# Performance work log

Hardware: AMD Instinct MI355X
Metric: run time of the kernel (lower is better)

Reference implementation:

```python
import jax, jax.numpy as jnp
import numpy as np

GROUPS = 8

def conv1d(x, w, b, stride=1, groups=1):
    # x: [B,C,L], w: [O, I//groups, K]
    y = jax.lax.conv_general_dilated(x, w, (stride,), 'VALID',
        dimension_numbers=('NCH', 'OIH', 'NCH'), feature_group_count=groups)
    return y + b[None, :, None]

def shuffle1d(x, groups):
    B, C, L = x.shape
    cpg = C // groups
    return x.reshape(B, groups, cpg, L).transpose(0, 2, 1, 3).reshape(B, C, L)

def setup_inputs() -> dict:
    key = jax.random.key(0)
    ks = jax.random.split(key, 12)
    C = 256
    B, L = 8, 4096
    g = GROUPS
    sc = 0.05
    inp = {
        'x':   jax.random.normal(ks[0], (B, C, L), dtype=jnp.float32),
        'w1':  jax.random.normal(ks[1], (C, C // g, 3), dtype=jnp.float32) * sc,
        'b1':  jax.random.normal(ks[2], (C,), dtype=jnp.float32) * sc,
        'w2':  jax.random.normal(ks[3], (C, C // g, 3), dtype=jnp.float32) * sc,
        'b2':  jax.random.normal(ks[4], (C,), dtype=jnp.float32) * sc,
        'wa1': jax.random.normal(ks[5], (C, 2 * C // g, 1), dtype=jnp.float32) * sc,
        'ba1': jax.random.normal(ks[6], (C,), dtype=jnp.float32) * sc,
        'wa2': jax.random.normal(ks[7], (C, C // g, 1), dtype=jnp.float32) * sc,
        'ba2': jax.random.normal(ks[8], (C,), dtype=jnp.float32) * sc,
        'w3':  jax.random.normal(ks[9], (C, C // g, 5), dtype=jnp.float32) * sc,  # kernel_size-4=5
        'b3':  jax.random.normal(ks[10], (C,), dtype=jnp.float32) * sc,
    }
    return inp

def reference(x, w1, b1, w2, b2, wa1, ba1, wa2, ba2, w3, b3):
    g = GROUPS
    # in_state has length 0 at init, so cat is identity; L >= kernel_size.
    h = conv1d(x, w1, b1, stride=1, groups=g)      # [B,C,L-2]
    h = shuffle1d(h, g)
    h = conv1d(h, w2, b2, stride=1, groups=g)      # [B,C,L-4]
    h = shuffle1d(h, g)
    # SortAttn: stable ascending sort over channel dim
    sorted_h = jnp.sort(h, axis=1, stable=True)
    a = conv1d(jnp.concatenate((sorted_h, h), axis=1), wa1, ba1, stride=1, groups=g)
    a = shuffle1d(a, g)
    a = jax.nn.sigmoid(conv1d(a, wa2, ba2, stride=1, groups=g))
    h = h * a
    y = conv1d(h, w3, b3, stride=1, groups=g)      # [B,C,L-8]
    return y
```

## Files before the change

### kernel.cpp

```cpp
#include <hip/hip_runtime.h>
#include <math.h>

#define BB 8
#define CCH 256
#define LLEN 4096
#define L1V 4094
#define L2V 4092
#define L3V 4088
#define NCOL (BB * L2V)

__global__ void prep_kernel(const float* __restrict__ wa1, const float* __restrict__ wa2,
                            float* __restrict__ wt1T, float* __restrict__ wt2T) {
    int i = blockIdx.x;
    int o = threadIdx.x;
    if (i < 64) {
        wt1T[i * 256 + o] = wa1[o * 64 + i];
    } else {
        int ii = i - 64;
        if (ii < 32) wt2T[ii * 256 + o] = wa2[o * 32 + ii];
    }
}

__global__ __launch_bounds__(256, 4) void conv1_kernel(const float* __restrict__ x,
                                                       const float* __restrict__ w1,
                                                       const float* __restrict__ b1,
                                                       float* __restrict__ t1) {
    __shared__ float xs[9248];
    const int b = blockIdx.y;
    const int l0 = blockIdx.x * 32;
    const int t = threadIdx.x;

#pragma unroll
    for (int j = 0; j < 9; ++j) {
        int f = t + 256 * j;
        int row = f / 9;
        int q = f - row * 9;
        size_t rb = (size_t)(b * CCH + row) * LLEN;
        float4 v;
        int base = l0 + 4 * q;
        if (base + 3 < LLEN) {
            v = *(const float4*)(x + rb + base);
        } else {
            v.x = x[rb + min(base + 0, LLEN - 1)];
            v.y = x[rb + min(base + 1, LLEN - 1)];
            v.z = x[rb + min(base + 2, LLEN - 1)];
            v.w = x[rb + min(base + 3, LLEN - 1)];
        }
        int a = row * 36 + (row >> 5) * 4 + 4 * q;
        *(float4*)&xs[a] = v;
    }
    __syncthreads();

    const int oc = t;
    const int go = t >> 5;
    float acc[32];
#pragma unroll
    for (int l = 0; l < 32; ++l) acc[l] = 0.f;

    for (int i = 0; i < 32; ++i) {
        int row = go * 32 + i;
        int base = row * 36 + go * 4;
        float wv0 = w1[oc * 96 + i * 3 + 0];
        float wv1 = w1[oc * 96 + i * 3 + 1];
        float wv2 = w1[oc * 96 + i * 3 + 2];
#pragma unroll
        for (int q = 0; q < 9; ++q) {
            float4 v = *(const float4*)&xs[base + 4 * q];
#pragma unroll
            for (int j = 0; j < 4; ++j) {
                int e = 4 * q + j;
                float xv = (&v.x)[j];
                if (e < 32) acc[e] += wv0 * xv;
                if (e >= 1 && e <= 32) acc[e - 1] += wv1 * xv;
                if (e >= 2 && e <= 33) acc[e - 2] += wv2 * xv;
            }
        }
    }
    float bias = b1[oc];
    int nc = (oc & 31) * 8 + (oc >> 5);
    float* dst = t1 + (size_t)(b * L1V + l0) * CCH + nc;
#pragma unroll
    for (int l = 0; l < 32; ++l) {
        if (l0 + l < L1V) dst[(size_t)l * CCH] = acc[l] + bias;
    }
}

__global__ __launch_bounds__(256, 4) void conv2_kernel(const float* __restrict__ t1,
                                                       const float* __restrict__ w2,
                                                       const float* __restrict__ b2,
                                                       float* __restrict__ t2) {
    __shared__ float ts[9792];
    const int b = blockIdx.y;
    const int l0 = blockIdx.x * 32;
    const int t = threadIdx.x;

#pragma unroll
    for (int j = 0; j < 9; ++j) {
        int f = t + 256 * j;
        if (f < 2176) {
            int p = f >> 6;
            int c4 = (f & 63) * 4;
            int row = min(l0 + p, L1V - 1);
            float4 v = *(const float4*)(t1 + (size_t)(b * L1V + row) * CCH + c4);
            *(float4*)&ts[p * 288 + (c4 >> 5) * 36 + (c4 & 31)] = v;
        }
    }
    __syncthreads();

    const int oc = t;
    const int go = t >> 5;
    float acc[32];
#pragma unroll
    for (int l = 0; l < 32; ++l) acc[l] = 0.f;

    for (int i4 = 0; i4 < 8; ++i4) {
        float wv[12];
#pragma unroll
        for (int z = 0; z < 12; ++z) wv[z] = w2[oc * 96 + i4 * 12 + z];
        int colbase = go * 36 + i4 * 4;
#pragma unroll
        for (int p = 0; p < 34; ++p) {
            float4 rv = *(const float4*)&ts[p * 288 + colbase];
#pragma unroll
            for (int cc = 0; cc < 4; ++cc) {
                float xv = (&rv.x)[cc];
#pragma unroll
                for (int k = 0; k < 3; ++k) {
                    int l = p - k;
                    if (l >= 0 && l < 32) acc[l] += wv[cc * 3 + k] * xv;
                }
            }
        }
    }
    float bias = b2[oc];
    int nc = (oc & 31) * 8 + (oc >> 5);
    float* dst = t2 + (size_t)(b * L2V + l0) * CCH + nc;
#pragma unroll
    for (int l = 0; l < 32; ++l) {
        if (l0 + l < L2V) dst[(size_t)l * CCH] = acc[l] + bias;
    }
}

__device__ __forceinline__ void ce_pair(float& a, float& b, bool up) {
    float lo = fminf(a, b), hi = fmaxf(a, b);
    a = up ? lo : hi;
    b = up ? hi : lo;
}

__device__ __forceinline__ void bitonic256(float v[4], int lane) {
#pragma unroll
    for (int k = 2; k <= 256; k <<= 1) {
#pragma unroll
        for (int j = k >> 1; j > 0; j >>= 1) {
            if (j >= 4) {
                int lm = j >> 2;
                bool upper = (lane & lm) != 0;
#pragma unroll
                for (int r = 0; r < 4; ++r) {
                    float other = __shfl_xor(v[r], lm, 64);
                    bool dirUp = (((4 * lane + r) & k) == 0);
                    bool keepMin = (dirUp != upper);
                    float lo = fminf(v[r], other), hi = fmaxf(v[r], other);
                    v[r] = keepMin ? lo : hi;
                }
            } else if (j == 2) {
#pragma unroll
                for (int r = 0; r < 2; ++r) {
                    bool up = (((4 * lane + r) & k) == 0);
                    ce_pair(v[r], v[r + 2], up);
                }
            } else {
#pragma unroll
                for (int r = 0; r < 4; r += 2) {
                    bool up = (((4 * lane + r) & k) == 0);
                    ce_pair(v[r], v[r + 1], up);
                }
            }
        }
    }
}

__global__ __launch_bounds__(256, 4) void attn_kernel(float* __restrict__ t2,
                                                      const float* __restrict__ wt1T,
                                                      const float* __restrict__ wt2T,
                                                      const float* __restrict__ ba1,
                                                      const float* __restrict__ ba2) {
    __shared__ float sm[8320];
    const int t = threadIdx.x;
    const int wv = t >> 6;
    const int lane = t & 63;
    const int wbase = wv * 2080;
    const int go = lane >> 3;

    float4 ba1v = *(const float4*)&ba1[4 * lane];
    float4 ba2v = *(const float4*)&ba2[4 * lane];

    const int colBase = blockIdx.x * 16 + wv * 4;

    float4 hv[4];
#pragma unroll
    for (int cc = 0; cc < 4; ++cc) {
        hv[cc] = *(const float4*)(t2 + (size_t)(colBase + cc) * CCH + 4 * lane);
    }
#pragma unroll
    for (int r = 0; r < 4; ++r) {
        int e = 4 * lane + r;
        int slot = ((e >> 6) + 4) * 65 + (e & 63);
        float4 vvv = make_float4((&hv[0].x)[r], (&hv[1].x)[r], (&hv[2].x)[r], (&hv[3].x)[r]);
        *(float4*)&sm[wbase + slot * 4] = vvv;
    }
    float srt[4][4];
#pragma unroll
    for (int cc = 0; cc < 4; ++cc) {
        float s[4] = {hv[cc].x, hv[cc].y, hv[cc].z, hv[cc].w};
        bitonic256(s, lane);
        srt[cc][0] = s[0]; srt[cc][1] = s[1]; srt[cc][2] = s[2]; srt[cc][3] = s[3];
    }
#pragma unroll
    for (int r = 0; r < 4; ++r) {
        int e = 4 * lane + r;
        int slot = (e >> 6) * 65 + (e & 63);
        float4 vvv = make_float4(srt[0][r], srt[1][r], srt[2][r], srt[3][r]);
        *(float4*)&sm[wbase + slot * 4] = vvv;
    }

    float4 acc[4];
#pragma unroll
    for (int cc = 0; cc < 4; ++cc) acc[cc] = make_float4(0.f, 0.f, 0.f, 0.f);
#pragma unroll 4
    for (int i = 0; i < 64; ++i) {
        float4 w4 = *(const float4*)&wt1T[i * 256 + 4 * lane];
        float4 cv = *(const float4*)&sm[wbase + (go * 65 + i) * 4];
#pragma unroll
        for (int cc = 0; cc < 4; ++cc) {
            float cvv = (&cv.x)[cc];
            acc[cc].x += w4.x * cvv;
            acc[cc].y += w4.y * cvv;
            acc[cc].z += w4.z * cvv;
            acc[cc].w += w4.w * cvv;
        }
    }
#pragma unroll
    for (int r = 0; r < 4; ++r) {
        float bb = (&ba1v.x)[r];
        float4 vvv = make_float4((&acc[0].x)[r] + bb, (&acc[1].x)[r] + bb,
                                 (&acc[2].x)[r] + bb, (&acc[3].x)[r] + bb);
        *(float4*)&sm[wbase + (5 * lane + r) * 4] = vvv;
    }

    float4 acc2[4];
#pragma unroll
    for (int cc = 0; cc < 4; ++cc) acc2[cc] = make_float4(0.f, 0.f, 0.f, 0.f);
#pragma unroll 4
    for (int i = 0; i < 32; ++i) {
        float4 w4 = *(const float4*)&wt2T[i * 256 + 4 * lane];
        int idx = ((i & 7) << 5) + (go << 2) + (i >> 3);
        int slotA = idx + (idx >> 2);
        float4 av = *(const float4*)&sm[wbase + slotA * 4];
#pragma unroll
        for (int cc = 0; cc < 4; ++cc) {
            float avv = (&av.x)[cc];
            acc2[cc].x += w4.x * avv;
            acc2[cc].y += w4.y * avv;
            acc2[cc].z += w4.z * avv;
            acc2[cc].w += w4.w * avv;
        }
    }
#pragma unroll
    for (int cc = 0; cc < 4; ++cc) {
        float zx = acc2[cc].x + ba2v.x;
        float zy = acc2[cc].y + ba2v.y;
        float zz = acc2[cc].z + ba2v.z;
        float zw = acc2[cc].w + ba2v.w;
        float4 res;
        res.x = hv[cc].x * (1.f / (1.f + __expf(-zx)));
        res.y = hv[cc].y * (1.f / (1.f + __expf(-zy)));
        res.z = hv[cc].z * (1.f / (1.f + __expf(-zz)));
        res.w = hv[cc].w * (1.f / (1.f + __expf(-zw)));
        *(float4*)(t2 + (size_t)(colBase + cc) * CCH + 4 * lane) = res;
    }
}

__global__ __launch_bounds__(256, 4) void conv3_kernel(const float* __restrict__ hm,
                                                       const float* __restrict__ w3,
                                                       const float* __restrict__ b3,
                                                       float* __restrict__ out) {
    __shared__ float ts[10368];
    const int b = blockIdx.y;
    const int l0 = blockIdx.x * 32;
    const int t = threadIdx.x;

#pragma unroll
    for (int j = 0; j < 9; ++j) {
        int f = t + 256 * j;
        int p = f >> 6;
        int c4 = (f & 63) * 4;
        int row = min(l0 + p, L2V - 1);
        float4 v = *(const float4*)(hm + (size_t)(b * L2V + row) * CCH + c4);
        *(float4*)&ts[p * 288 + (c4 >> 5) * 36 + (c4 & 31)] = v;
    }
    __syncthreads();

    const int oc = t;
    const int go = t >> 5;
    float acc[32];
#pragma unroll
    for (int l = 0; l < 32; ++l) acc[l] = 0.f;

    for (int i4 = 0; i4 < 8; ++i4) {
        float wv[20];
#pragma unroll
        for (int z = 0; z < 20; ++z) wv[z] = w3[oc * 160 + i4 * 20 + z];
        int colbase = go * 36 + i4 * 4;
#pragma unroll
        for (int p = 0; p < 36; ++p) {
            float4 rv = *(const float4*)&ts[p * 288 + colbase];
#pragma unroll
            for (int cc = 0; cc < 4; ++cc) {
                float xv = (&rv.x)[cc];
#pragma unroll
                for (int k = 0; k < 5; ++k) {
                    int l = p - k;
                    if (l >= 0 && l < 32) acc[l] += wv[cc * 5 + k] * xv;
                }
            }
        }
    }
    float bias = b3[oc];
    float* dst = out + (size_t)(b * CCH + oc) * L3V + l0;
#pragma unroll
    for (int l4 = 0; l4 < 8; ++l4) {
        int gl = l0 + 4 * l4;
        if (gl + 3 < L3V) {
            float4 v;
            v.x = acc[4 * l4 + 0] + bias;
            v.y = acc[4 * l4 + 1] + bias;
            v.z = acc[4 * l4 + 2] + bias;
            v.w = acc[4 * l4 + 3] + bias;
            *(float4*)(dst + 4 * l4) = v;
        } else {
#pragma unroll
            for (int c = 0; c < 4; ++c) {
                if (gl + c < L3V) dst[4 * l4 + c] = acc[4 * l4 + c] + bias;
            }
        }
    }
}

extern "C" void kernel_launch(void* const* d_in, const int* in_sizes, int n_in,
                              void* d_out, int out_size, void* d_ws, size_t ws_size,
                              hipStream_t stream) {
    const float* x   = (const float*)d_in[0];
    const float* w1  = (const float*)d_in[1];
    const float* b1  = (const float*)d_in[2];
    const float* w2  = (const float*)d_in[3];
    const float* b2  = (const float*)d_in[4];
    const float* wa1 = (const float*)d_in[5];
    const float* ba1 = (const float*)d_in[6];
    const float* wa2 = (const float*)d_in[7];
    const float* ba2 = (const float*)d_in[8];
    const float* w3  = (const float*)d_in[9];
    const float* b3  = (const float*)d_in[10];
    float* out = (float*)d_out;

    char* ws = (char*)d_ws;
    float* t1   = (float*)ws;
    float* t2   = (float*)(ws + ((size_t)32 << 20));
    float* wt1T = (float*)(ws + ((size_t)64 << 20));
    float* wt2T = wt1T + 64 * 256;

    hipLaunchKernelGGL(prep_kernel, dim3(96), dim3(256), 0, stream, wa1, wa2, wt1T, wt2T);
    hipLaunchKernelGGL(conv1_kernel, dim3(128, BB), dim3(256), 0, stream, x, w1, b1, t1);
    hipLaunchKernelGGL(conv2_kernel, dim3(128, BB), dim3(256), 0, stream, t1, w2, b2, t2);
    hipLaunchKernelGGL(attn_kernel, dim3(2046), dim3(256), 0, stream, t2, wt1T, wt2T, ba1, ba2);
    hipLaunchKernelGGL(conv3_kernel, dim3(128, BB), dim3(256), 0, stream, t2, w3, b3, out);
}
```

Before: 298.8 us.

## Fuse conv1 and conv2 into one kernel with shared-memory intermediate

Merges the first two grouped convolutions into a single kernel. Each block computes 34 positions of conv1 (a 2-element halo), writes them shuffled into shared memory, then runs conv2 from there, so the t1 round trip through global memory and one launch go away. The conv2 output is staged in shared memory and written back as coalesced float4 rows. Weight loads in conv12 and conv3 become float4 loads that are software-prefetched one chunk ahead. The cost is a slightly larger conv1 accumulator and extra syncs.

```diff
diff --git a/kernel.cpp b/kernel.cpp
--- a/kernel.cpp
+++ b/kernel.cpp
@@ -8,6 +8,7 @@
 #define L2V 4092
 #define L3V 4088
 #define NCOL (BB * L2V)
+#define PIT 260
 
 __global__ void prep_kernel(const float* __restrict__ wa1, const float* __restrict__ wa2,
                             float* __restrict__ wt1T, float* __restrict__ wt2T) {
@@ -21,10 +22,12 @@
     }
 }
 
-__global__ __launch_bounds__(256, 4) void conv1_kernel(const float* __restrict__ x,
-                                                       const float* __restrict__ w1,
-                                                       const float* __restrict__ b1,
-                                                       float* __restrict__ t1) {
+__global__ __launch_bounds__(256, 4) void conv12_kernel(const float* __restrict__ x,
+                                                        const float* __restrict__ w1,
+                                                        const float* __restrict__ b1,
+                                                        const float* __restrict__ w2,
+                                                        const float* __restrict__ b2,
+                                                        float* __restrict__ t2) {
     __shared__ float xs[9248];
     const int b = blockIdx.y;
     const int l0 = blockIdx.x * 32;
@@ -36,8 +39,8 @@
         int row = f / 9;
         int q = f - row * 9;
         size_t rb = (size_t)(b * CCH + row) * LLEN;
+        int base = l0 + 4 * q;
         float4 v;
-        int base = l0 + 4 * q;
         if (base + 3 < LLEN) {
             v = *(const float4*)(x + rb + base);
         } else {
@@ -46,98 +49,99 @@
             v.z = x[rb + min(base + 2, LLEN - 1)];
             v.w = x[rb + min(base + 3, LLEN - 1)];
         }
-        int a = row * 36 + (row >> 5) * 4 + 4 * q;
-        *(float4*)&xs[a] = v;
+        *(float4*)&xs[row * 36 + (row >> 5) * 4 + 4 * q] = v;
     }
     __syncthreads();
 
     const int oc = t;
-    const int go = t >> 5;
-    float acc[32];
-#pragma unroll
-    for (int l = 0; l < 32; ++l) acc[l] = 0.f;
-
-    for (int i = 0; i < 32; ++i) {
-        int row = go * 32 + i;
-        int base = row * 36 + go * 4;
-        float wv0 = w1[oc * 96 + i * 3 + 0];
-        float wv1 = w1[oc * 96 + i * 3 + 1];
-        float wv2 = w1[oc * 96 + i * 3 + 2];
-#pragma unroll
-        for (int q = 0; q < 9; ++q) {
-            float4 v = *(const float4*)&xs[base + 4 * q];
-#pragma unroll
-            for (int j = 0; j < 4; ++j) {
-                int e = 4 * q + j;
-                float xv = (&v.x)[j];
-                if (e < 32) acc[e] += wv0 * xv;
-                if (e >= 1 && e <= 32) acc[e - 1] += wv1 * xv;
-                if (e >= 2 && e <= 33) acc[e - 2] += wv2 * xv;
-            }
-        }
-    }
-    float bias = b1[oc];
-    int nc = (oc & 31) * 8 + (oc >> 5);
-    float* dst = t1 + (size_t)(b * L1V + l0) * CCH + nc;
-#pragma unroll
-    for (int l = 0; l < 32; ++l) {
-        if (l0 + l < L1V) dst[(size_t)l * CCH] = acc[l] + bias;
-    }
-}
-
-__global__ __launch_bounds__(256, 4) void conv2_kernel(const float* __restrict__ t1,
-                                                       const float* __restrict__ w2,
-                                                       const float* __restrict__ b2,
-                                                       float* __restrict__ t2) {
-    __shared__ float ts[9792];
-    const int b = blockIdx.y;
-    const int l0 = blockIdx.x * 32;
-    const int t = threadIdx.x;
-
-#pragma unroll
-    for (int j = 0; j < 9; ++j) {
-        int f = t + 256 * j;
-        if (f < 2176) {
-            int p = f >> 6;
-            int c4 = (f & 63) * 4;
-            int row = min(l0 + p, L1V - 1);
-            float4 v = *(const float4*)(t1 + (size_t)(b * L1V + row) * CCH + c4);
-            *(float4*)&ts[p * 288 + (c4 >> 5) * 36 + (c4 & 31)] = v;
-        }
-    }
-    __syncthreads();
-
-    const int oc = t;
-    const int go = t >> 5;
-    float acc[32];
-#pragma unroll
-    for (int l = 0; l < 32; ++l) acc[l] = 0.f;
-
-    for (int i4 = 0; i4 < 8; ++i4) {
-        float wv[12];
-#pragma unroll
-        for (int z = 0; z < 12; ++z) wv[z] = w2[oc * 96 + i4 * 12 + z];
-        int colbase = go * 36 + i4 * 4;
-#pragma unroll
-        for (int p = 0; p < 34; ++p) {
-            float4 rv = *(const float4*)&ts[p * 288 + colbase];
-#pragma unroll
-            for (int cc = 0; cc < 4; ++cc) {
-                float xv = (&rv.x)[cc];
-#pragma unroll
-                for (int k = 0; k < 3; ++k) {
-                    int l = p - k;
-                    if (l >= 0 && l < 32) acc[l] += wv[cc * 3 + k] * xv;
-                }
-            }
-        }
-    }
-    float bias = b2[oc];
-    int nc = (oc & 31) * 8 + (oc >> 5);
-    float* dst = t2 + (size_t)(b * L2V + l0) * CCH + nc;
-#pragma unroll
-    for (int l = 0; l < 32; ++l) {
-        if (l0 + l < L2V) dst[(size_t)l * CCH] = acc[l] + bias;
+    const int go = oc >> 5;
+    const int nc = (oc & 31) * 8 + (oc >> 5);
+
+    float acc1[34];
+#pragma unroll
+    for (int l = 0; l < 34; ++l) acc1[l] = 0.f;
+    {
+        const float4* wrow = (const float4*)(w1 + oc * 96);
+        float4 wc0 = wrow[0], wc1 = wrow[1], wc2 = wrow[2];
+        for (int ch = 0; ch < 8; ++ch) {
+            float4 wn0 = wrow[min(3 * ch + 3, 23)];
+            float4 wn1 = wrow[min(3 * ch + 4, 23)];
+            float4 wn2 = wrow[min(3 * ch + 5, 23)];
+            float wf[12];
+            *(float4*)&wf[0] = wc0; *(float4*)&wf[4] = wc1; *(float4*)&wf[8] = wc2;
+#pragma unroll
+            for (int ii = 0; ii < 4; ++ii) {
+                int row = go * 32 + ch * 4 + ii;
+                int base = row * 36 + go * 4;
+                float w0 = wf[ii * 3 + 0], w1v = wf[ii * 3 + 1], w2v = wf[ii * 3 + 2];
+#pragma unroll
+                for (int q = 0; q < 9; ++q) {
+                    float4 v = *(const float4*)&xs[base + 4 * q];
+#pragma unroll
+                    for (int jj = 0; jj < 4; ++jj) {
+                        int e = 4 * q + jj;
+                        float xv = (&v.x)[jj];
+                        if (e < 34) acc1[e] += w0 * xv;
+                        if (e >= 1 && e <= 34) acc1[e - 1] += w1v * xv;
+                        if (e >= 2 && e <= 35) acc1[e - 2] += w2v * xv;
+                    }
+                }
+            }
+            wc0 = wn0; wc1 = wn1; wc2 = wn2;
+        }
+    }
+    float bias1 = b1[oc];
+    __syncthreads();
+
+#pragma unroll
+    for (int l = 0; l < 34; ++l) xs[l * PIT + nc] = acc1[l] + bias1;
+    __syncthreads();
+
+    float acc2[32];
+#pragma unroll
+    for (int l = 0; l < 32; ++l) acc2[l] = 0.f;
+    {
+        const float4* wrow = (const float4*)(w2 + oc * 96);
+        float4 wc0 = wrow[0], wc1 = wrow[1], wc2 = wrow[2];
+        for (int i4 = 0; i4 < 8; ++i4) {
+            float4 wn0 = wrow[min(3 * i4 + 3, 23)];
+            float4 wn1 = wrow[min(3 * i4 + 4, 23)];
+            float4 wn2 = wrow[min(3 * i4 + 5, 23)];
+            float wf[12];
+            *(float4*)&wf[0] = wc0; *(float4*)&wf[4] = wc1; *(float4*)&wf[8] = wc2;
+            int colbase = go * 32 + i4 * 4;
+#pragma unroll
+            for (int p = 0; p < 34; ++p) {
+                float4 rv = *(const float4*)&xs[p * PIT + colbase];
+#pragma unroll
+                for (int cc = 0; cc < 4; ++cc) {
+                    float xv = (&rv.x)[cc];
+#pragma unroll
+                    for (int k = 0; k < 3; ++k) {
+                        int l = p - k;
+                        if (l >= 0 && l < 32) acc2[l] += wf[cc * 3 + k] * xv;
+                    }
+                }
+            }
+            wc0 = wn0; wc1 = wn1; wc2 = wn2;
+        }
+    }
+    float bias2 = b2[oc];
+    __syncthreads();
+
+#pragma unroll
+    for (int l = 0; l < 32; ++l) xs[l * PIT + nc] = acc2[l] + bias2;
+    __syncthreads();
+
+#pragma unroll
+    for (int j = 0; j < 8; ++j) {
+        int idx = t + 256 * j;
+        int row = idx >> 6;
+        int c4 = (idx & 63) * 4;
+        if (l0 + row < L2V) {
+            float4 v = *(const float4*)&xs[row * PIT + c4];
+            *(float4*)(t2 + (size_t)(b * L2V + l0 + row) * CCH + c4) = v;
+        }
     }
 }
 
@@ -307,23 +311,33 @@
 #pragma unroll
     for (int l = 0; l < 32; ++l) acc[l] = 0.f;
 
-    for (int i4 = 0; i4 < 8; ++i4) {
-        float wv[20];
-#pragma unroll
-        for (int z = 0; z < 20; ++z) wv[z] = w3[oc * 160 + i4 * 20 + z];
-        int colbase = go * 36 + i4 * 4;
-#pragma unroll
-        for (int p = 0; p < 36; ++p) {
-            float4 rv = *(const float4*)&ts[p * 288 + colbase];
-#pragma unroll
-            for (int cc = 0; cc < 4; ++cc) {
-                float xv = (&rv.x)[cc];
-#pragma unroll
-                for (int k = 0; k < 5; ++k) {
-                    int l = p - k;
-                    if (l >= 0 && l < 32) acc[l] += wv[cc * 5 + k] * xv;
-                }
-            }
+    {
+        const float4* wrow = (const float4*)(w3 + oc * 160);
+        float4 wc0 = wrow[0], wc1 = wrow[1], wc2 = wrow[2], wc3 = wrow[3], wc4 = wrow[4];
+        for (int i4 = 0; i4 < 8; ++i4) {
+            float4 wn0 = wrow[min(5 * i4 + 5, 39)];
+            float4 wn1 = wrow[min(5 * i4 + 6, 39)];
+            float4 wn2 = wrow[min(5 * i4 + 7, 39)];
+            float4 wn3 = wrow[min(5 * i4 + 8, 39)];
+            float4 wn4 = wrow[min(5 * i4 + 9, 39)];
+            float wf[20];
+            *(float4*)&wf[0] = wc0; *(float4*)&wf[4] = wc1; *(float4*)&wf[8] = wc2;
+            *(float4*)&wf[12] = wc3; *(float4*)&wf[16] = wc4;
+            int colbase = go * 36 + i4 * 4;
+#pragma unroll
+            for (int p = 0; p < 36; ++p) {
+                float4 rv = *(const float4*)&ts[p * 288 + colbase];
+#pragma unroll
+                for (int cc = 0; cc < 4; ++cc) {
+                    float xv = (&rv.x)[cc];
+#pragma unroll
+                    for (int k = 0; k < 5; ++k) {
+                        int l = p - k;
+                        if (l >= 0 && l < 32) acc[l] += wf[cc * 5 + k] * xv;
+                    }
+                }
+            }
+            wc0 = wn0; wc1 = wn1; wc2 = wn2; wc3 = wn3; wc4 = wn4;
         }
     }
     float bias = b3[oc];
@@ -364,14 +378,12 @@
     float* out = (float*)d_out;
 
     char* ws = (char*)d_ws;
-    float* t1   = (float*)ws;
-    float* t2   = (float*)(ws + ((size_t)32 << 20));
-    float* wt1T = (float*)(ws + ((size_t)64 << 20));
+    float* t2   = (float*)ws;
+    float* wt1T = (float*)(ws + ((size_t)48 << 20));
     float* wt2T = wt1T + 64 * 256;
 
     hipLaunchKernelGGL(prep_kernel, dim3(96), dim3(256), 0, stream, wa1, wa2, wt1T, wt2T);
-    hipLaunchKernelGGL(conv1_kernel, dim3(128, BB), dim3(256), 0, stream, x, w1, b1, t1);
-    hipLaunchKernelGGL(conv2_kernel, dim3(128, BB), dim3(256), 0, stream, t1, w2, b2, t2);
+    hipLaunchKernelGGL(conv12_kernel, dim3(128, BB), dim3(256), 0, stream, x, w1, b1, w2, b2, t2);
     hipLaunchKernelGGL(attn_kernel, dim3(2046), dim3(256), 0, stream, t2, wt1T, wt2T, ba1, ba2);
     hipLaunchKernelGGL(conv3_kernel, dim3(128, BB), dim3(256), 0, stream, t2, w3, b3, out);
 }
```

Result: slower. 503.2 us (+68.4%).
